# Optimization experiments

Measured on AMD Instinct MI355X. Metric: run time of the kernel, lower is better.

## Reference

```python
import jax, jax.numpy as jnp
import numpy as np

A = 5            # num_anchors
NC = 20          # num_classes
IGNORE_THRESH = 0.6
COORD_SCALE = 1.0
NOOBJ_SCALE = 1.0
OBJ_SCALE = 5.0
CLASS_SCALE = 1.0
ANCHORS_NP = np.array([[0.052, 0.066], [0.14, 0.11], [0.24, 0.30], [0.45, 0.42], [0.77, 0.72]], dtype=np.float32)


def setup_inputs() -> dict:
    key = jax.random.key(0)
    k1, k2, k3, k4, k5 = jax.random.split(key, 5)
    B, F, O = 32, 38, 50
    C = A * (5 + NC)
    outputs = jax.random.normal(k1, (B, C, F, F), jnp.float32)
    # targets: (cx, cy, w, h, cls) normalized; padded rows are all-zero
    cxy = jax.random.uniform(k2, (B, O, 2), minval=0.15, maxval=0.85)
    wh = jax.random.uniform(k3, (B, O, 2), minval=0.05, maxval=0.20)
    cls = jax.random.randint(k4, (B, O), 0, NC).astype(jnp.float32)
    targets = jnp.concatenate([cxy, wh, cls[..., None]], axis=-1)
    nobj = jax.random.randint(k5, (B,), 10, O + 1)
    valid = (jnp.arange(O)[None, :] < nobj[:, None]).astype(jnp.float32)
    targets = targets * valid[..., None]
    return {"outputs": outputs, "targets": targets, "anchors": jnp.asarray(ANCHORS_NP)}


def _pairwise_iou_xywh(a, b):
    # a: (..., N, 4), b: (..., M, 4) center-format -> IoU (..., N, M)
    a = a[..., :, None, :]
    b = b[..., None, :, :]
    tl = jnp.maximum(a[..., :2] - a[..., 2:] * 0.5, b[..., :2] - b[..., 2:] * 0.5)
    br = jnp.minimum(a[..., :2] + a[..., 2:] * 0.5, b[..., :2] + b[..., 2:] * 0.5)
    wh = jnp.clip(br - tl, 0.0)
    inter = wh[..., 0] * wh[..., 1]
    area_a = a[..., 2] * a[..., 3]
    area_b = b[..., 2] * b[..., 3]
    return inter / (area_a + area_b - inter + 1e-12)


def _forward(outputs, targets, anchors):
    B, C, F, _ = outputs.shape
    S = F * F
    O = targets.shape[1]
    valid = targets.sum(axis=2) > 0                    # (B, O)
    gt = targets[..., :4] * F                          # grid-unit cxywh
    gt_cls = targets[..., 4]

    out5 = outputs.reshape(B, A, 5 + NC, F, F)
    jj = jnp.arange(F, dtype=outputs.dtype)            # x (last axis)
    ii = jnp.arange(F, dtype=outputs.dtype)[:, None]   # y
    aw = (anchors[:, 0] * F)[None, :, None, None]
    ah = (anchors[:, 1] * F)[None, :, None, None]
    px = jax.nn.sigmoid(out5[:, :, 0]) + jj
    py = jax.nn.sigmoid(out5[:, :, 1]) + ii
    pw = jnp.exp(out5[:, :, 2]) * aw
    ph = jnp.exp(out5[:, :, 3]) * ah
    pred_boxes = jnp.stack([px, py, pw, ph], -1).transpose(0, 2, 3, 1, 4).reshape(B, S * A, 4)

    # anchor prior boxes at cell centers: (S, A, 4)
    ax = jnp.broadcast_to(jj + 0.5, (F, F))
    ay = jnp.broadcast_to(ii + 0.5, (F, F))
    aa = jnp.stack([
        jnp.broadcast_to(ax[:, :, None], (F, F, A)),
        jnp.broadcast_to(ay[:, :, None], (F, F, A)),
        jnp.broadcast_to((anchors[:, 0] * F)[None, None, :], (F, F, A)),
        jnp.broadcast_to((anchors[:, 1] * F)[None, None, :], (F, F, A)),
    ], -1).reshape(S, A, 4)

    ious = _pairwise_iou_xywh(pred_boxes, gt)          # (B, S*A, O)
    ious = jnp.where(valid[:, None, :], ious, 0.0)     # padded objs excluded (IoU >= 0)
    max_iou = ious.reshape(B, S, A, O).max(axis=-1)    # (B, S, A)

    n_pos = jnp.any(max_iou > IGNORE_THRESH, axis=(1, 2))
    iou_mask = jnp.full((B, S, A), NOOBJ_SCALE, outputs.dtype)
    iou_mask = jnp.where(n_pos[:, None, None] & (max_iou >= IGNORE_THRESH), 0.0, iou_mask)

    overlaps = _pairwise_iou_xywh(aa.reshape(1, S * A, 4), gt).reshape(B, S, A, O)

    # responsible cell: floor of top-left corner (faithful to source), anchor = argmax prior overlap
    x1y1 = gt[..., :2] - gt[..., 2:] * 0.5
    cxcy = jnp.floor(x1y1).astype(jnp.int32)
    cell = jnp.clip(cxcy[..., 1] * F + cxcy[..., 0], 0, S - 1)             # (B, O)
    ovT = overlaps.transpose(0, 3, 1, 2)                                   # (B, O, S, A)
    ov_cell = jnp.take_along_axis(ovT, cell[:, :, None, None], axis=2)[:, :, 0, :]
    anchor_idx = jnp.argmax(ov_cell, axis=-1)                              # (B, O)
    resp = aa[cell, anchor_idx]                                            # (B, O, 4)
    deltas = jnp.stack([gt[..., 0] - resp[..., 0], gt[..., 1] - resp[..., 1],
                        gt[..., 2] / resp[..., 2], gt[..., 3] / resp[..., 3]], -1)
    mi = jnp.take_along_axis(jnp.take_along_axis(max_iou, cell[:, :, None], axis=1),
                             anchor_idx[:, :, None], axis=2)[..., 0]       # (B, O)

    b_rep = jnp.broadcast_to(jnp.arange(B)[:, None], (B, O))
    cell_s = jnp.where(valid, cell, S)  # OOB index for padded objs -> dropped
    zt = jnp.zeros((B, S, A), outputs.dtype)
    box_target = jnp.zeros((B, S, A, 4), outputs.dtype).at[b_rep, cell_s, anchor_idx].set(deltas, mode='drop')
    box_mask = zt.at[b_rep, cell_s, anchor_idx].set(1.0, mode='drop')
    class_target = zt.at[b_rep, cell_s, anchor_idx].set(gt_cls, mode='drop')
    class_mask = zt.at[b_rep, cell_s, anchor_idx].set(1.0, mode='drop')
    iou_target = zt.at[b_rep, cell_s, anchor_idx].set(mi, mode='drop')
    iou_mask = iou_mask.at[b_rep, cell_s, anchor_idx].set(OBJ_SCALE, mode='drop')

    # prediction side, layout (B, (i*F+j)*A + a, 5+NC) matching target layout
    outs = out5.transpose(0, 3, 4, 1, 2).reshape(B, S * A, 5 + NC)
    pd = jnp.concatenate([jax.nn.sigmoid(outs[..., :2]), jnp.exp(outs[..., 2:4])], -1)
    conf = jax.nn.sigmoid(outs[..., 4])
    probs = jax.nn.softmax(outs[..., 5:], axis=-1)

    bm = box_mask.reshape(B, S * A, 1)
    im = iou_mask.reshape(B, S * A)
    box_loss = jnp.sum((pd * bm - box_target.reshape(B, S * A, 4) * bm) ** 2)
    iou_loss = jnp.sum((conf * im - iou_target.reshape(B, S * A) * im) ** 2)
    # faithful quirk of the source: cross-entropy applied to softmax *outputs* as logits
    ls = jax.nn.log_softmax(probs, axis=-1)
    ct = class_target.reshape(B, S * A).astype(jnp.int32)
    ce = -jnp.take_along_axis(ls, ct[..., None], axis=-1)[..., 0]
    class_loss = jnp.sum(ce * class_mask.reshape(B, S * A))
    return (COORD_SCALE * box_loss + iou_loss + CLASS_SCALE * class_loss) / B


def reference(outputs, targets, anchors):
    return _forward(outputs, targets, anchors)
```

## Files before the change

### kernel.cpp

```cpp
#include <hip/hip_runtime.h>
#include <math.h>

#define A_N 5
#define NC 20
#define FD 38
#define SD (FD*FD)
#define BD 32
#define OD 50
#define SA (SD*A_N)
#define HALF (SA/2)
#define GXP 15
#define SLOTB 16
#define NSLOT (BD * SLOTB)
#define IGN_T 0.6f
#define OBJ_S 5.0f

__device__ __forceinline__ float sigm(float x) { return 1.0f / (1.0f + __expf(-x)); }

__global__ __launch_bounds__(256, 6) void k_main(
    const float* __restrict__ outputs, const float* __restrict__ targets,
    const float* __restrict__ anchors,
    float* __restrict__ pbase, float* __restrict__ pcorr, int* __restrict__ pflag)
{
    __shared__ float4 g_box[OD];
    __shared__ float  g_den[OD];
    __shared__ float  s_anc[2 * A_N];
    __shared__ int    s_cnt, s_any;
    __shared__ int    s_key[OD];
    __shared__ float  wb[4], wc[4];

    const int b = blockIdx.y;
    const int tid = threadIdx.x;
    if (tid == 0) { s_cnt = 0; s_any = 0; }
    if (tid < 2 * A_N) s_anc[tid] = anchors[tid];

    if (blockIdx.x == GXP) {
        __syncthreads();
        float gx = 0, gy = 0, gw = 0, gh = 0;
        int ct = 0, key = -1;
        if (tid < OD) {
            const float* t = targets + (b * OD + tid) * 5;
            float tx = t[0], ty = t[1], tw = t[2], th = t[3], tc = t[4];
            if (tx + ty + tw + th + tc > 0.0f) {
                gx = tx * FD; gy = ty * FD; gw = tw * FD; gh = th * FD;
                float gtlx = gx - gw*0.5f, gtly = gy - gh*0.5f;
                float gbrx = gx + gw*0.5f, gbry = gy + gh*0.5f;
                int k = atomicAdd(&s_cnt, 1);
                g_box[k] = make_float4(gtlx, gtly, gbrx, gbry);
                g_den[k] = gw * gh + 1e-12f;
                int cx = (int)floorf(gtlx), cy = (int)floorf(gtly);
                int cell = min(max(cy * FD + cx, 0), SD - 1);
                int ci = cell / FD, cj = cell - ci * FD;
                float acx = (float)cj + 0.5f, acy = (float)ci + 0.5f;
                float areaB = gw * gh;
                float best = -1.0f; int bi = 0;
                for (int a = 0; a < A_N; ++a) {
                    float aw = s_anc[2*a] * FD, ah = s_anc[2*a+1] * FD;
                    float w = fmaxf(fminf(acx + aw*0.5f, gbrx) - fmaxf(acx - aw*0.5f, gtlx), 0.0f);
                    float h = fmaxf(fminf(acy + ah*0.5f, gbry) - fmaxf(acy - ah*0.5f, gtly), 0.0f);
                    float inter = w * h;
                    float iou = inter / (aw*ah + areaB - inter + 1e-12f);
                    if (iou > best) { best = iou; bi = a; }
                }
                key = bi * SD + cell;
                ct = (int)tc;
            }
        }
        if (tid < OD) s_key[tid] = key;
        __syncthreads();
        const int cnt = s_cnt;

        float rbase = 0.0f, rcorr = 0.0f;
        if (tid < OD && key >= 0) {
            int win = -1;
            #pragma unroll 10
            for (int o = 0; o < OD; ++o) win = (s_key[o] == key) ? o : win;
            if (win == tid) {
                int a = key / SD, cell = key - a * SD;
                int ci = cell / FD, cj = cell - ci * FD;
                const float* ob = outputs + ((size_t)b * (A_N * 25) + a * 25) * SD + cell;
                float o0 = ob[0], o1 = ob[SD], o2 = ob[2*SD], o3 = ob[3*SD], o4 = ob[4*SD];
                float aw = s_anc[2*a] * FD, ah = s_anc[2*a+1] * FD;
                float px = sigm(o0) + (float)cj;
                float py = sigm(o1) + (float)ci;
                float ew = __expf(o2), eh = __expf(o3);
                float pw = ew * aw, ph = eh * ah;
                float tlx = px - pw*0.5f, tly = py - ph*0.5f;
                float brx = px + pw*0.5f, bry = py + ph*0.5f;
                float ar = pw * ph;
                float bn = 0.0f, bd = 1.0f;
                for (int o = 0; o < cnt; ++o) {
                    float4 bx = g_box[o];
                    float w = fmaxf(fminf(brx, bx.z) - fmaxf(tlx, bx.x), 0.0f);
                    float h = fmaxf(fminf(bry, bx.w) - fmaxf(tly, bx.y), 0.0f);
                    float in = w * h, de = ar + g_den[o] - in;
                    if (in * bd > bn * de) { bn = in; bd = de; }
                }
                float mi = bn / bd;
                float conf = sigm(o4);
                float d = conf - mi;
                rbase += OBJ_S * OBJ_S * d * d;
                float c2 = conf * conf;
                if (bn >= IGN_T * bd) rcorr -= c2;
                else                  rbase -= c2;
                float dx = gx - ((float)cj + 0.5f);
                float dy = gy - ((float)ci + 0.5f);
                float e0 = sigm(o0) - dx;
                float e1 = sigm(o1) - dy;
                float e2 = ew - gw / aw;
                float e3 = eh - gh / ah;
                rbase += e0*e0 + e1*e1 + e2*e2 + e3*e3;
                const float* cb = ob + 5 * SD;
                float xmax = -INFINITY;
                #pragma unroll
                for (int k = 0; k < NC; ++k) xmax = fmaxf(xmax, cb[k * SD]);
                float esum = 0.0f;
                #pragma unroll
                for (int k = 0; k < NC; ++k) esum += __expf(cb[k * SD] - xmax);
                float inv = 1.0f / esum;
                float pmax = inv;
                float pct = __expf(cb[ct * SD] - xmax) * inv;
                float e2s = 0.0f;
                #pragma unroll
                for (int k = 0; k < NC; ++k)
                    e2s += __expf(__expf(cb[k * SD] - xmax) * inv - pmax);
                rbase += -(pct - (pmax + __logf(e2s)));
            }
        }
        #pragma unroll
        for (int off = 32; off > 0; off >>= 1) {
            rbase += __shfl_down(rbase, off);
            rcorr += __shfl_down(rcorr, off);
        }
        int lane = tid & 63, w = tid >> 6;
        if (lane == 0) { wb[w] = rbase; wc[w] = rcorr; }
        __syncthreads();
        if (tid == 0) {
            int gid = b * SLOTB + GXP;
            pbase[gid] = wb[0] + wb[1] + wb[2] + wb[3];
            pcorr[gid] = wc[0] + wc[1] + wc[2] + wc[3];
            pflag[gid] = 0;
        }
        return;
    }

    const int ix = blockIdx.x * 256 + tid;
    const bool act = (ix < HALF);
    const int p0 = ix, p1 = ix + HALF;
    int a0 = p0 / SD, r0 = p0 - a0 * SD;
    int a1 = p1 / SD, r1 = p1 - a1 * SD;
    int ii0 = r0 / FD, jj0 = r0 - ii0 * FD;
    int ii1 = r1 / FD, jj1 = r1 - ii1 * FD;
    const float* ob0 = outputs + ((size_t)b * (A_N * 25) + a0 * 25) * SD + r0;
    const float* ob1 = outputs + ((size_t)b * (A_N * 25) + a1 * 25) * SD + r1;
    float q00 = 0, q01 = 0, q02 = 0, q03 = 0, q04 = 0;
    float q10 = 0, q11 = 0, q12 = 0, q13 = 0, q14 = 0;
    if (act) {
        q00 = ob0[0]; q01 = ob0[SD]; q02 = ob0[2*SD]; q03 = ob0[3*SD]; q04 = ob0[4*SD];
        q10 = ob1[0]; q11 = ob1[SD]; q12 = ob1[2*SD]; q13 = ob1[3*SD]; q14 = ob1[4*SD];
    }
    if (tid < OD) {
        const float* t = targets + (b * OD + tid) * 5;
        float tx = t[0], ty = t[1], tw = t[2], th = t[3], tc = t[4];
        if (tx + ty + tw + th + tc > 0.0f) {
            float gx = tx * FD, gy = ty * FD, gw = tw * FD, gh = th * FD;
            int k = atomicAdd(&s_cnt, 1);
            g_box[k] = make_float4(gx - gw*0.5f, gy - gh*0.5f, gx + gw*0.5f, gy + gh*0.5f);
            g_den[k] = gw * gh + 1e-12f;
        }
    }
    __syncthreads();
    const int cnt = s_cnt;

    float base = 0.0f, corr = 0.0f;
    bool hot = false;
    if (act) {
        float aw0 = s_anc[2*a0] * FD, ah0 = s_anc[2*a0+1] * FD;
        float aw1 = s_anc[2*a1] * FD, ah1 = s_anc[2*a1+1] * FD;
        float px0 = sigm(q00) + (float)jj0, py0 = sigm(q01) + (float)ii0;
        float px1 = sigm(q10) + (float)jj1, py1 = sigm(q11) + (float)ii1;
        float pw0 = __expf(q02) * aw0, ph0 = __expf(q03) * ah0;
        float pw1 = __expf(q12) * aw1, ph1 = __expf(q13) * ah1;
        float tlx0 = px0 - pw0*0.5f, tly0 = py0 - ph0*0.5f;
        float brx0 = px0 + pw0*0.5f, bry0 = py0 + ph0*0.5f;
        float tlx1 = px1 - pw1*0.5f, tly1 = py1 - ph1*0.5f;
        float brx1 = px1 + pw1*0.5f, bry1 = py1 + ph1*0.5f;
        float ar0 = pw0 * ph0, ar1 = pw1 * ph1;

        float bn0 = 0.0f, bd0 = 1.0f, bn1 = 0.0f, bd1 = 1.0f;
        for (int o = 0; o < cnt; ++o) {
            float4 bx = g_box[o];
            float dn = g_den[o];
            float w0 = fmaxf(fminf(brx0, bx.z) - fmaxf(tlx0, bx.x), 0.0f);
            float h0 = fmaxf(fminf(bry0, bx.w) - fmaxf(tly0, bx.y), 0.0f);
            float in0 = w0 * h0, de0 = ar0 + dn - in0;
            if (in0 * bd0 > bn0 * de0) { bn0 = in0; bd0 = de0; }
            float w1 = fmaxf(fminf(brx1, bx.z) - fmaxf(tlx1, bx.x), 0.0f);
            float h1 = fmaxf(fminf(bry1, bx.w) - fmaxf(tly1, bx.y), 0.0f);
            float in1 = w1 * h1, de1 = ar1 + dn - in1;
            if (in1 * bd1 > bn1 * de1) { bn1 = in1; bd1 = de1; }
        }
        float t0 = IGN_T * bd0, t1 = IGN_T * bd1;
        hot = (bn0 > t0) || (bn1 > t1);
        float c0 = sigm(q04); c0 *= c0;
        float c1 = sigm(q14); c1 *= c1;
        if (bn0 >= t0) corr += c0; else base += c0;
        if (bn1 >= t1) corr += c1; else base += c1;
    }

    unsigned long long bal = __ballot(hot);
    if ((tid & 63) == 0 && bal) atomicOr(&s_any, 1);

    #pragma unroll
    for (int off = 32; off > 0; off >>= 1) {
        base += __shfl_down(base, off);
        corr += __shfl_down(corr, off);
    }
    int lane = tid & 63, w = tid >> 6;
    if (lane == 0) { wb[w] = base; wc[w] = corr; }
    __syncthreads();
    if (tid == 0) {
        int gid = b * SLOTB + blockIdx.x;
        pbase[gid] = wb[0] + wb[1] + wb[2] + wb[3];
        pcorr[gid] = wc[0] + wc[1] + wc[2] + wc[3];
        pflag[gid] = s_any;
    }
}

__global__ __launch_bounds__(256) void k_fin(
    const float* __restrict__ pbase, const float* __restrict__ pcorr,
    const int* __restrict__ pflag, float* __restrict__ out)
{
    __shared__ int npos[BD];
    __shared__ float wsum[4];
    const int tid = threadIdx.x;
    if (tid < BD) {
        int f = 0;
        for (int x = 0; x < SLOTB; ++x) f |= pflag[tid * SLOTB + x];
        npos[tid] = f;
    }
    __syncthreads();
    float s = 0.0f;
    for (int g = tid; g < NSLOT; g += 256)
        s += pbase[g] + (npos[g >> 4] ? 0.0f : pcorr[g]);
    #pragma unroll
    for (int off = 32; off > 0; off >>= 1) s += __shfl_down(s, off);
    int lane = tid & 63, w = tid >> 6;
    if (lane == 0) wsum[w] = s;
    __syncthreads();
    if (tid == 0) out[0] = (wsum[0] + wsum[1] + wsum[2] + wsum[3]) * (1.0f / (float)BD);
}

extern "C" void kernel_launch(void* const* d_in, const int* in_sizes, int n_in,
                              void* d_out, int out_size, void* d_ws, size_t ws_size,
                              hipStream_t stream) {
    (void)in_sizes; (void)n_in; (void)out_size; (void)ws_size;
    const float* outputs = (const float*)d_in[0];
    const float* targets = (const float*)d_in[1];
    const float* anchors = (const float*)d_in[2];
    float* out = (float*)d_out;

    float* pbase = (float*)d_ws;
    float* pcorr = pbase + NSLOT;
    int*   pflag = (int*)(pcorr + NSLOT);

    k_main<<<dim3(GXP + 1, BD), 256, 0, stream>>>(outputs, targets, anchors,
                                                  pbase, pcorr, pflag);
    k_fin<<<dim3(1), 256, 0, stream>>>(pbase, pcorr, pflag, out);
}
```

Measured before the change: 77.81 us.

## Use one anchor per thread with a division-free IoU threshold test

Each thread now handles one anchor-cell instead of two, which doubles the grid to 29 compute blocks per batch. The inner IoU loop drops the tracked best-ratio comparison. It instead takes the maximum of a linear threshold expression, (1+t)*inter - t*areaB - t*areaP, which removes the per-box cross-multiplied compare and bookkeeping. Ground-truth compaction uses a wavefront ballot and popcount instead of shared-memory atomics, which gives a deterministic order. The occupancy hint in launch bounds is removed, and there are more blocks and finalization slots to reduce.

Result: slower. 81.12 us (+4.3%).

```diff
diff --git a/kernel.cpp b/kernel.cpp
--- a/kernel.cpp
+++ b/kernel.cpp
@@ -8,22 +8,21 @@
 #define BD 32
 #define OD 50
 #define SA (SD*A_N)
-#define HALF (SA/2)
-#define GXP 15
-#define SLOTB 16
+#define GXP 29
+#define SLOTB 30
 #define NSLOT (BD * SLOTB)
 #define IGN_T 0.6f
 #define OBJ_S 5.0f
 
 __device__ __forceinline__ float sigm(float x) { return 1.0f / (1.0f + __expf(-x)); }
 
-__global__ __launch_bounds__(256, 6) void k_main(
+__global__ __launch_bounds__(256) void k_main(
     const float* __restrict__ outputs, const float* __restrict__ targets,
     const float* __restrict__ anchors,
     float* __restrict__ pbase, float* __restrict__ pcorr, int* __restrict__ pflag)
 {
     __shared__ float4 g_box[OD];
-    __shared__ float  g_den[OD];
+    __shared__ float  g_e[OD];
     __shared__ float  s_anc[2 * A_N];
     __shared__ int    s_cnt, s_any;
     __shared__ int    s_key[OD];
@@ -31,10 +30,11 @@
 
     const int b = blockIdx.y;
     const int tid = threadIdx.x;
-    if (tid == 0) { s_cnt = 0; s_any = 0; }
+    if (tid == 0) s_any = 0;
     if (tid < 2 * A_N) s_anc[tid] = anchors[tid];
 
     if (blockIdx.x == GXP) {
+        if (tid == 0) s_cnt = 0;
         __syncthreads();
         float gx = 0, gy = 0, gw = 0, gh = 0;
         int ct = 0, key = -1;
@@ -47,7 +47,7 @@
                 float gbrx = gx + gw*0.5f, gbry = gy + gh*0.5f;
                 int k = atomicAdd(&s_cnt, 1);
                 g_box[k] = make_float4(gtlx, gtly, gbrx, gbry);
-                g_den[k] = gw * gh + 1e-12f;
+                g_e[k] = gw * gh + 1e-12f;
                 int cx = (int)floorf(gtlx), cy = (int)floorf(gtly);
                 int cell = min(max(cy * FD + cx, 0), SD - 1);
                 int ci = cell / FD, cj = cell - ci * FD;
@@ -93,7 +93,7 @@
                     float4 bx = g_box[o];
                     float w = fmaxf(fminf(brx, bx.z) - fmaxf(tlx, bx.x), 0.0f);
                     float h = fmaxf(fminf(bry, bx.w) - fmaxf(tly, bx.y), 0.0f);
-                    float in = w * h, de = ar + g_den[o] - in;
+                    float in = w * h, de = ar + g_e[o] - in;
                     if (in * bd > bn * de) { bn = in; bd = de; }
                 }
                 float mi = bn / bd;
@@ -144,30 +144,35 @@
         return;
     }
 
-    const int ix = blockIdx.x * 256 + tid;
-    const bool act = (ix < HALF);
-    const int p0 = ix, p1 = ix + HALF;
-    int a0 = p0 / SD, r0 = p0 - a0 * SD;
-    int a1 = p1 / SD, r1 = p1 - a1 * SD;
-    int ii0 = r0 / FD, jj0 = r0 - ii0 * FD;
-    int ii1 = r1 / FD, jj1 = r1 - ii1 * FD;
-    const float* ob0 = outputs + ((size_t)b * (A_N * 25) + a0 * 25) * SD + r0;
-    const float* ob1 = outputs + ((size_t)b * (A_N * 25) + a1 * 25) * SD + r1;
-    float q00 = 0, q01 = 0, q02 = 0, q03 = 0, q04 = 0;
-    float q10 = 0, q11 = 0, q12 = 0, q13 = 0, q14 = 0;
-    if (act) {
-        q00 = ob0[0]; q01 = ob0[SD]; q02 = ob0[2*SD]; q03 = ob0[3*SD]; q04 = ob0[4*SD];
-        q10 = ob1[0]; q11 = ob1[SD]; q12 = ob1[2*SD]; q13 = ob1[3*SD]; q14 = ob1[4*SD];
-    }
-    if (tid < OD) {
-        const float* t = targets + (b * OD + tid) * 5;
-        float tx = t[0], ty = t[1], tw = t[2], th = t[3], tc = t[4];
-        if (tx + ty + tw + th + tc > 0.0f) {
-            float gx = tx * FD, gy = ty * FD, gw = tw * FD, gh = th * FD;
-            int k = atomicAdd(&s_cnt, 1);
-            g_box[k] = make_float4(gx - gw*0.5f, gy - gh*0.5f, gx + gw*0.5f, gy + gh*0.5f);
-            g_den[k] = gw * gh + 1e-12f;
-        }
+    const int idx = blockIdx.x * 256 + tid;
+    const bool act = (idx < SA);
+    const int a = idx / SD, s = idx - a * SD;
+    const int i = s / FD, j = s - i * FD;
+    const float* ob = outputs + ((size_t)b * (A_N * 25) + a * 25) * SD + s;
+    float q0 = 0, q1 = 0, q2 = 0, q3 = 0, q4 = 0;
+    if (act) { q0 = ob[0]; q1 = ob[SD]; q2 = ob[2*SD]; q3 = ob[3*SD]; q4 = ob[4*SD]; }
+
+    if (tid < 64) {
+        bool v = false;
+        float gtlx = 0, gtly = 0, gbrx = 0, gbry = 0, e = 0;
+        if (tid < OD) {
+            const float* t = targets + (b * OD + tid) * 5;
+            float tx = t[0], ty = t[1], tw = t[2], th = t[3], tc = t[4];
+            if (tx + ty + tw + th + tc > 0.0f) {
+                v = true;
+                float gx = tx * FD, gy = ty * FD, gw = tw * FD, gh = th * FD;
+                gtlx = gx - gw*0.5f; gtly = gy - gh*0.5f;
+                gbrx = gx + gw*0.5f; gbry = gy + gh*0.5f;
+                e = IGN_T * (gw * gh + 1e-12f);
+            }
+        }
+        unsigned long long bal = __ballot(v);
+        if (v) {
+            int k = __popcll(bal & ((1ull << tid) - 1ull));
+            g_box[k] = make_float4(gtlx, gtly, gbrx, gbry);
+            g_e[k] = e;
+        }
+        if (tid == 0) s_cnt = __popcll(bal);
     }
     __syncthreads();
     const int cnt = s_cnt;
@@ -175,37 +180,28 @@
     float base = 0.0f, corr = 0.0f;
     bool hot = false;
     if (act) {
-        float aw0 = s_anc[2*a0] * FD, ah0 = s_anc[2*a0+1] * FD;
-        float aw1 = s_anc[2*a1] * FD, ah1 = s_anc[2*a1+1] * FD;
-        float px0 = sigm(q00) + (float)jj0, py0 = sigm(q01) + (float)ii0;
-        float px1 = sigm(q10) + (float)jj1, py1 = sigm(q11) + (float)ii1;
-        float pw0 = __expf(q02) * aw0, ph0 = __expf(q03) * ah0;
-        float pw1 = __expf(q12) * aw1, ph1 = __expf(q13) * ah1;
-        float tlx0 = px0 - pw0*0.5f, tly0 = py0 - ph0*0.5f;
-        float brx0 = px0 + pw0*0.5f, bry0 = py0 + ph0*0.5f;
-        float tlx1 = px1 - pw1*0.5f, tly1 = py1 - ph1*0.5f;
-        float brx1 = px1 + pw1*0.5f, bry1 = py1 + ph1*0.5f;
-        float ar0 = pw0 * ph0, ar1 = pw1 * ph1;
-
-        float bn0 = 0.0f, bd0 = 1.0f, bn1 = 0.0f, bd1 = 1.0f;
+        float aw = s_anc[2*a] * FD, ah = s_anc[2*a+1] * FD;
+        float px = sigm(q0) + (float)j;
+        float py = sigm(q1) + (float)i;
+        float pw = __expf(q2) * aw;
+        float ph = __expf(q3) * ah;
+        float tlx = px - pw*0.5f, tly = py - ph*0.5f;
+        float brx = px + pw*0.5f, bry = py + ph*0.5f;
+        float f6 = IGN_T * (pw * ph);
+
+        float dmax = -1e30f;
         for (int o = 0; o < cnt; ++o) {
             float4 bx = g_box[o];
-            float dn = g_den[o];
-            float w0 = fmaxf(fminf(brx0, bx.z) - fmaxf(tlx0, bx.x), 0.0f);
-            float h0 = fmaxf(fminf(bry0, bx.w) - fmaxf(tly0, bx.y), 0.0f);
-            float in0 = w0 * h0, de0 = ar0 + dn - in0;
-            if (in0 * bd0 > bn0 * de0) { bn0 = in0; bd0 = de0; }
-            float w1 = fmaxf(fminf(brx1, bx.z) - fmaxf(tlx1, bx.x), 0.0f);
-            float h1 = fmaxf(fminf(bry1, bx.w) - fmaxf(tly1, bx.y), 0.0f);
-            float in1 = w1 * h1, de1 = ar1 + dn - in1;
-            if (in1 * bd1 > bn1 * de1) { bn1 = in1; bd1 = de1; }
-        }
-        float t0 = IGN_T * bd0, t1 = IGN_T * bd1;
-        hot = (bn0 > t0) || (bn1 > t1);
-        float c0 = sigm(q04); c0 *= c0;
-        float c1 = sigm(q14); c1 *= c1;
-        if (bn0 >= t0) corr += c0; else base += c0;
-        if (bn1 >= t1) corr += c1; else base += c1;
+            float w = fmaxf(fminf(brx, bx.z) - fmaxf(tlx, bx.x), 0.0f);
+            float h = fmaxf(fminf(bry, bx.w) - fmaxf(tly, bx.y), 0.0f);
+            float in = w * h;
+            float d = (1.0f + IGN_T) * in - g_e[o] - f6;
+            dmax = fmaxf(dmax, d);
+        }
+        hot = (dmax > 0.0f);
+        float c2 = sigm(q4); c2 *= c2;
+        if (dmax >= 0.0f) corr += c2;
+        else              base += c2;
     }
 
     unsigned long long bal = __ballot(hot);
@@ -242,7 +238,7 @@
     __syncthreads();
     float s = 0.0f;
     for (int g = tid; g < NSLOT; g += 256)
-        s += pbase[g] + (npos[g >> 4] ? 0.0f : pcorr[g]);
+        s += pbase[g] + (npos[g / SLOTB] ? 0.0f : pcorr[g]);
     #pragma unroll
     for (int off = 32; off > 0; off >>= 1) s += __shfl_down(s, off);
     int lane = tid & 63, w = tid >> 6;
```
